# Kernel tuning notes

Hardware: AMD Instinct MI355X
Metric: run time of the kernel (lower is better)

The kernel has to match this reference:

```python
import jax, jax.numpy as jnp
import numpy as np


def setup_inputs() -> dict:
    key = jax.random.key(0)
    k1, k2 = jax.random.split(key)
    B, T, D = 32, 1024, 384
    encodings = jax.random.normal(k1, (B, T, D), dtype=jnp.float32)
    durations = jax.random.randint(k2, (B, T), 0, 8, dtype=jnp.int32)
    return {"encodings": encodings, "durations": durations}


def reference(encodings, durations):
    # encodings: [B, T, D] float; durations: [B, T] int (torch code rounds .item())
    B, T, D = encodings.shape
    reps = jnp.round(durations).astype(jnp.int32)            # [B, T]
    csum = jnp.cumsum(reps, axis=1)                          # [B, T] exclusive end offsets
    totals = csum[:, -1]                                     # [B] expanded length per batch
    # max_len computed from concrete durations (dynamic output length, like the torch code)
    max_len = int(jnp.max(totals))
    pos = jnp.arange(max_len)                                # [L]
    # frame p belongs to token j where csum[j-1] <= p < csum[j] -> searchsorted right
    idx = jax.vmap(lambda c: jnp.searchsorted(c, pos, side="right"))(csum)  # [B, L]
    idx = jnp.minimum(idx, T - 1)
    out = jnp.take_along_axis(encodings, idx[:, :, None], axis=1)           # [B, L, D]
    mask = pos[None, :] < totals[:, None]                                   # [B, L]
    return jnp.where(mask[:, :, None], out, jnp.zeros((), dtype=encodings.dtype))
```

## Files before the change

### kernel.cpp

```cpp
#include <hip/hip_runtime.h>

#define NB 32
#define NT 1024
#define ND 384
#define ND4 (ND / 4)
#define FPW 4
#define WPB 4
#define FPB (FPW * WPB)

typedef float vfloat4 __attribute__((ext_vector_type(4)));

__global__ void __launch_bounds__(NT)
scan_pad_kernel(const int* __restrict__ dur,
                int* __restrict__ csum,
                vfloat4* __restrict__ out,
                int max_len) {
    __shared__ int wsum[16];
    const int b = blockIdx.x;
    const int t = threadIdx.x;
    const int lane = t & 63;
    const int w = t >> 6;
    const int d = dur[b * NT + t];

    int x = d;
    #pragma unroll
    for (int off = 1; off < 64; off <<= 1) {
        int y = __shfl_up(x, off, 64);
        if (lane >= off) x += y;
    }
    if (lane == 63) wsum[w] = x;
    __syncthreads();
    if (w == 0) {
        int v = (lane < 16) ? wsum[lane] : 0;
        #pragma unroll
        for (int off = 1; off < 16; off <<= 1) {
            int y = __shfl_up(v, off, 64);
            if (lane >= off) v += y;
        }
        if (lane < 16) wsum[lane] = v;
    }
    __syncthreads();
    const int c = x + (w ? wsum[w - 1] : 0);
    const int total = wsum[15];
    csum[b * NT + t] = c;

    vfloat4* out_b = out + (size_t)b * max_len * ND4;
    const vfloat4 z = {0.f, 0.f, 0.f, 0.f};
    const int end = max_len * ND4;
    for (int i = total * ND4 + t; i < end; i += NT)
        __builtin_nontemporal_store(z, &out_b[i]);
}

__global__ void __launch_bounds__(256)
expand_kernel(const vfloat4* __restrict__ enc,
              const int* __restrict__ csum,
              vfloat4* __restrict__ out,
              int max_len) {
    const int b = blockIdx.y;
    const int lane = threadIdx.x & 63;
    const int wv = threadIdx.x >> 6;
    const int f0 = blockIdx.x * FPB + wv * FPW;

    const int* csum_b = csum + b * NT;
    const vfloat4* enc_b = enc + (size_t)b * NT * ND4;
    vfloat4* out_b = out + (size_t)b * (size_t)max_len * ND4;

    int e[FPW], s[FPW];
    #pragma unroll
    for (int k = 0; k < FPW; ++k)
        e[k] = csum_b[f0 + k];
    s[0] = f0 ? csum_b[f0 - 1] : 0;
    #pragma unroll
    for (int k = 1; k < FPW; ++k)
        s[k] = e[k - 1];

    vfloat4 v0[FPW], v1[FPW];
    #pragma unroll
    for (int k = 0; k < FPW; ++k) {
        const vfloat4* src = enc_b + (size_t)(f0 + k) * ND4;
        v0[k] = src[lane];
        if (lane < 32) v1[k] = src[64 + lane];
    }

    #pragma unroll
    for (int k = 0; k < FPW; ++k) {
        for (int p = s[k]; p < e[k]; ++p) {
            vfloat4* dst = out_b + (size_t)p * ND4;
            __builtin_nontemporal_store(v0[k], dst + lane);
            if (lane < 32)
                __builtin_nontemporal_store(v1[k], dst + 64 + lane);
        }
    }
}

extern "C" void kernel_launch(void* const* d_in, const int* in_sizes, int n_in,
                              void* d_out, int out_size, void* d_ws, size_t ws_size,
                              hipStream_t stream) {
    const float* enc = (const float*)d_in[0];
    const int*   dur = (const int*)d_in[1];
    float* out = (float*)d_out;

    const int max_len = out_size / (NB * ND);

    int* csum = (int*)d_ws;

    scan_pad_kernel<<<NB, NT, 0, stream>>>(dur, csum, (vfloat4*)out, max_len);

    dim3 grid(NT / FPB, NB);
    expand_kernel<<<grid, 256, 0, stream>>>(
        (const vfloat4*)enc, csum, (vfloat4*)out, max_len);
}
```

Baseline: 225.2 us.

## Fuse scan and expand into one kernel with per-block redundant prefix sum

The separate scan/pad kernel is removed. Each expand block now recomputes the per-batch cumulative sum in shared memory from vectorized duration loads, which eliminates one launch and the global csum round trip. Padding zeros are spread across all blocks of a batch. Frames are written two at a time as three full-wave stores, and the stores become regular instead of nontemporal. In exchange, every block repeats the 1024-element scan, which is 64 times redundant per batch.

```diff
diff --git a/kernel.cpp b/kernel.cpp
--- a/kernel.cpp
+++ b/kernel.cpp
@@ -7,90 +7,96 @@
 #define FPW 4
 #define WPB 4
 #define FPB (FPW * WPB)
+#define NBX (NT / FPB)
+#define THREADS 256
 
 typedef float vfloat4 __attribute__((ext_vector_type(4)));
+typedef int   vint4   __attribute__((ext_vector_type(4)));
 
-__global__ void __launch_bounds__(NT)
-scan_pad_kernel(const int* __restrict__ dur,
-                int* __restrict__ csum,
-                vfloat4* __restrict__ out,
-                int max_len) {
-    __shared__ int wsum[16];
-    const int b = blockIdx.x;
-    const int t = threadIdx.x;
+__global__ void __launch_bounds__(THREADS)
+fused_expand_kernel(const vfloat4* __restrict__ enc,
+                    const int* __restrict__ dur,
+                    vfloat4* __restrict__ out,
+                    int max_len) {
+    __shared__ int sm_csum[NT];
+    __shared__ int wsum[WPB];
+
+    const int b    = blockIdx.y;
+    const int bx   = blockIdx.x;
+    const int t    = threadIdx.x;
     const int lane = t & 63;
-    const int w = t >> 6;
-    const int d = dur[b * NT + t];
+    const int wv   = t >> 6;
 
-    int x = d;
+    vint4 d4 = *(const vint4*)(dur + b * NT + 4 * t);
+    const int l0 = d4.x;
+    const int l1 = l0 + d4.y;
+    const int l2 = l1 + d4.z;
+    const int l3 = l2 + d4.w;
+    const int S  = l3;
+
+    int x = S;
     #pragma unroll
     for (int off = 1; off < 64; off <<= 1) {
         int y = __shfl_up(x, off, 64);
         if (lane >= off) x += y;
     }
-    if (lane == 63) wsum[w] = x;
+    if (lane == 63) wsum[wv] = x;
     __syncthreads();
-    if (w == 0) {
-        int v = (lane < 16) ? wsum[lane] : 0;
+    if (t == 0) {
+        int a = 0;
         #pragma unroll
-        for (int off = 1; off < 16; off <<= 1) {
-            int y = __shfl_up(v, off, 64);
-            if (lane >= off) v += y;
-        }
-        if (lane < 16) wsum[lane] = v;
+        for (int i = 0; i < WPB; ++i) { a += wsum[i]; wsum[i] = a; }
     }
     __syncthreads();
-    const int c = x + (w ? wsum[w - 1] : 0);
-    const int total = wsum[15];
-    csum[b * NT + t] = c;
+    const int P = (wv ? wsum[wv - 1] : 0) + (x - S);
+    sm_csum[4 * t + 0] = P + l0;
+    sm_csum[4 * t + 1] = P + l1;
+    sm_csum[4 * t + 2] = P + l2;
+    sm_csum[4 * t + 3] = P + l3;
+    const int total = wsum[WPB - 1];
+    __syncthreads();
 
-    vfloat4* out_b = out + (size_t)b * max_len * ND4;
-    const vfloat4 z = {0.f, 0.f, 0.f, 0.f};
-    const int end = max_len * ND4;
-    for (int i = total * ND4 + t; i < end; i += NT)
-        __builtin_nontemporal_store(z, &out_b[i]);
-}
+    const int f0 = bx * FPB + wv * FPW;
+    const vfloat4* enc_b = enc + (size_t)b * NT * ND4;
+    vfloat4*       out_b = out + (size_t)b * (size_t)max_len * ND4;
 
-__global__ void __launch_bounds__(256)
-expand_kernel(const vfloat4* __restrict__ enc,
-              const int* __restrict__ csum,
-              vfloat4* __restrict__ out,
-              int max_len) {
-    const int b = blockIdx.y;
-    const int lane = threadIdx.x & 63;
-    const int wv = threadIdx.x >> 6;
-    const int f0 = blockIdx.x * FPB + wv * FPW;
-
-    const int* csum_b = csum + b * NT;
-    const vfloat4* enc_b = enc + (size_t)b * NT * ND4;
-    vfloat4* out_b = out + (size_t)b * (size_t)max_len * ND4;
-
-    int e[FPW], s[FPW];
+    const int s0 = (f0 == 0) ? 0 : sm_csum[f0 - 1];
+    int e[FPW];
     #pragma unroll
     for (int k = 0; k < FPW; ++k)
-        e[k] = csum_b[f0 + k];
-    s[0] = f0 ? csum_b[f0 - 1] : 0;
-    #pragma unroll
-    for (int k = 1; k < FPW; ++k)
-        s[k] = e[k - 1];
+        e[k] = sm_csum[f0 + k];
 
-    vfloat4 v0[FPW], v1[FPW];
+    const int i1 = (lane < 32) ? (64 + lane) : (lane - 32);
+    vfloat4 v0[FPW], v1[FPW], v2[FPW];
     #pragma unroll
     for (int k = 0; k < FPW; ++k) {
         const vfloat4* src = enc_b + (size_t)(f0 + k) * ND4;
         v0[k] = src[lane];
-        if (lane < 32) v1[k] = src[64 + lane];
+        v1[k] = src[i1];
+        v2[k] = src[32 + lane];
     }
 
     #pragma unroll
     for (int k = 0; k < FPW; ++k) {
-        for (int p = s[k]; p < e[k]; ++p) {
+        int p = (k == 0) ? s0 : e[k - 1];
+        const int ee = e[k];
+        for (; p + 2 <= ee; p += 2) {
             vfloat4* dst = out_b + (size_t)p * ND4;
-            __builtin_nontemporal_store(v0[k], dst + lane);
-            if (lane < 32)
-                __builtin_nontemporal_store(v1[k], dst + 64 + lane);
+            dst[lane]        = v0[k];
+            dst[64 + lane]   = v1[k];
+            dst[128 + lane]  = v2[k];
+        }
+        if (p < ee) {
+            vfloat4* dst = out_b + (size_t)p * ND4;
+            dst[lane] = v0[k];
+            if (lane < 32) dst[64 + lane] = v1[k];
         }
     }
+
+    const int end4 = max_len * ND4;
+    const vfloat4 z = {0.f, 0.f, 0.f, 0.f};
+    for (int i = total * ND4 + bx * THREADS + t; i < end4; i += NBX * THREADS)
+        out_b[i] = z;
 }
 
 extern "C" void kernel_launch(void* const* d_in, const int* in_sizes, int n_in,
@@ -102,11 +108,7 @@
 
     const int max_len = out_size / (NB * ND);
 
-    int* csum = (int*)d_ws;
-
-    scan_pad_kernel<<<NB, NT, 0, stream>>>(dur, csum, (vfloat4*)out, max_len);
-
-    dim3 grid(NT / FPB, NB);
-    expand_kernel<<<grid, 256, 0, stream>>>(
-        (const vfloat4*)enc, csum, (vfloat4*)out, max_len);
+    dim3 grid(NBX, NB);
+    fused_expand_kernel<<<grid, THREADS, 0, stream>>>(
+        (const vfloat4*)enc, dur, (vfloat4*)out, max_len);
 }
```

Result: faster. 219.6 us (-2.5%).
